# Kernel tuning notes

Measured on AMD Instinct MI355X. Metric: run time of the kernel, lower is better.

The kernel has to match this reference:

```python
import jax, jax.numpy as jnp
import numpy as np

N_NODES = 10000
N_EDGES = 320000
D_FEAT = 512
N_HIDDEN = 256
N_LATENT = 64


def setup_inputs() -> dict:
    key = jax.random.key(0)
    ks = jax.random.split(key, 7)
    x = jax.random.normal(ks[0], (N_NODES, D_FEAT), dtype=jnp.float32)
    edge_src = jax.random.randint(ks[1], (N_EDGES,), 0, N_NODES, dtype=jnp.int32)
    edge_dst = jax.random.randint(ks[2], (N_EDGES,), 0, N_NODES, dtype=jnp.int32)
    # positive weights, like D^{-1/2} A D^{-1/2} entries
    edge_weight = jax.random.uniform(ks[3], (N_EDGES,), dtype=jnp.float32)
    scale1 = 1.0 / np.sqrt(D_FEAT)
    scale2 = 1.0 / np.sqrt(N_HIDDEN)
    W1 = jax.random.normal(ks[4], (D_FEAT, N_HIDDEN), dtype=jnp.float32) * scale1
    W2_mu = jax.random.normal(ks[5], (N_HIDDEN, N_LATENT), dtype=jnp.float32) * scale2
    W2_sig = jax.random.normal(ks[6], (N_HIDDEN, N_LATENT), dtype=jnp.float32) * scale2
    return {"x": x, "edge_src": edge_src, "edge_dst": edge_dst,
            "edge_weight": edge_weight, "W1": W1, "W2_mu": W2_mu, "W2_sig": W2_sig}


def reference(x, edge_src, edge_dst, edge_weight, W1, W2_mu, W2_sig):
    N = x.shape[0]

    def spmm(feat):
        # sparse adj_norm @ feat via gather + weighted segment-sum
        msg = feat[edge_src] * edge_weight[:, None]           # [E, F]
        return jax.ops.segment_sum(msg, edge_dst, num_segments=N)  # [N, F]

    # GCN layer 1: relu(adj @ (x @ W1)); dropout is identity at inference
    h = jax.nn.relu(spmm(x @ W1))                              # [N, H]
    # GCN layer 2 (mu and log-sigma heads); encoder returns exp(log_sig)
    mu = spmm(h @ W2_mu)                                       # [N, L]
    sigma = jnp.exp(spmm(h @ W2_sig))                          # [N, L]
    # InnerProductDecoder: adj = z @ z.T (normalized z_ is computed but unused
    # in the original code, so it is faithfully omitted); z = mu embedding
    adj_rec = mu @ mu.T                                        # [N, N]
    return mu, sigma, adj_rec
```

## Files before the change

kernel.cpp:

```cpp
#include <hip/hip_runtime.h>
#include <hip/hip_bf16.h>
#include <math.h>
#include <float.h>

#define N_NODES 10000
#define N_EDGES 320000
#define D_FEAT  512
#define N_HID   256
#define N_LAT   64

typedef __bf16 bf16x2 __attribute__((ext_vector_type(2)));
typedef __bf16 bf16x4 __attribute__((ext_vector_type(4)));
typedef __bf16 bf16x8 __attribute__((ext_vector_type(8)));
typedef float  f32x2  __attribute__((ext_vector_type(2)));
typedef float  f32x4  __attribute__((ext_vector_type(4)));


__global__ __launch_bounds__(256) void k_hist8(const int* __restrict__ dst,
                                               int* __restrict__ deg8) {
    int i = blockIdx.x * 256 + threadIdx.x;
    int sh = blockIdx.x & 7;
    if (i < N_EDGES) atomicAdd(&deg8[sh * N_NODES + dst[i]], 1);
}

__global__ __launch_bounds__(1024) void k_scan8(const int* __restrict__ deg8,
                                                int* __restrict__ rowptr,
                                                int* __restrict__ woff8) {
    __shared__ int wsum[16];
    __shared__ int carry_s;
    int tid = threadIdx.x;
    if (tid == 0) carry_s = 0;
    __syncthreads();
    int lane = tid & 63, wv = tid >> 6;
    for (int base = 0; base < N_NODES; base += 1024) {
        int i = base + tid;
        int d8[8];
        int v = 0;
        #pragma unroll
        for (int s = 0; s < 8; s++) {
            d8[s] = (i < N_NODES) ? deg8[s * N_NODES + i] : 0;
            v += d8[s];
        }
        int x = v;
        #pragma unroll
        for (int off = 1; off < 64; off <<= 1) {
            int y = __shfl_up(x, off);
            if (lane >= off) x += y;
        }
        if (lane == 63) wsum[wv] = x;
        __syncthreads();
        int add = carry_s;
        for (int k = 0; k < wv; k++) add += wsum[k];
        int incl = x + add;
        int excl = incl - v;
        if (i < N_NODES) {
            rowptr[i] = excl;
            int run = excl;
            #pragma unroll
            for (int s = 0; s < 8; s++) { woff8[s * N_NODES + i] = run; run += d8[s]; }
        }
        __syncthreads();
        if (tid == 1023) carry_s = incl;
        __syncthreads();
    }
    if (tid == 0) rowptr[N_NODES] = carry_s;
}

__global__ __launch_bounds__(256) void k_scatter8(const int* __restrict__ src,
                                                  const int* __restrict__ dst,
                                                  const float* __restrict__ w,
                                                  int* __restrict__ woff8,
                                                  int* __restrict__ esrc,
                                                  float* __restrict__ ew) {
    int i = blockIdx.x * 256 + threadIdx.x;
    int sh = blockIdx.x & 7;
    if (i < N_EDGES) {
        int d = dst[i];
        int r = atomicAdd(&woff8[sh * N_NODES + d], 1);
        esrc[r] = src[i];
        ew[r] = w[i];
    }
}


__global__ __launch_bounds__(256) void k_split(const float* __restrict__ x,
                                               const float* __restrict__ W1,
                                               const float* __restrict__ W2mu,
                                               const float* __restrict__ W2sig,
                                               __bf16* __restrict__ xh,
                                               __bf16* __restrict__ xl,
                                               __bf16* __restrict__ w1h,
                                               __bf16* __restrict__ w1l,
                                               __bf16* __restrict__ w2h,
                                               __bf16* __restrict__ w2l) {
    if (blockIdx.x < 5000) {
        int i = blockIdx.x * 256 + threadIdx.x;
        float4 v = ((const float4*)x)[i];
        __bf16 h0 = (__bf16)v.x, h1 = (__bf16)v.y, h2 = (__bf16)v.z, h3 = (__bf16)v.w;
        bf16x4 hv = {h0, h1, h2, h3};
        bf16x4 lv = {(__bf16)(v.x - (float)h0), (__bf16)(v.y - (float)h1),
                     (__bf16)(v.z - (float)h2), (__bf16)(v.w - (float)h3)};
        ((bf16x4*)xh)[i] = hv;
        ((bf16x4*)xl)[i] = lv;
    } else {
        int i = (blockIdx.x - 5000) * 256 + threadIdx.x;
        if (i < 512 * 256) {
            int j = i >> 9, k = i & 511;
            float v = W1[k * N_HID + j];
            __bf16 hi = (__bf16)v;
            w1h[i] = hi;
            w1l[i] = (__bf16)(v - (float)hi);
        } else {
            int t = i - 512 * 256;
            int j = t >> 8, k = t & 255;
            float v = (j < 64) ? W2mu[k * N_LAT + j] : W2sig[k * N_LAT + (j - 64)];
            __bf16 hi = (__bf16)v;
            w2h[t] = hi;
            w2l[t] = (__bf16)(v - (float)hi);
        }
    }
}


__global__ __launch_bounds__(256) void k_gemm1m(const __bf16* __restrict__ xh,
                                                const __bf16* __restrict__ xl,
                                                const __bf16* __restrict__ w1h,
                                                const __bf16* __restrict__ w1l,
                                                float* __restrict__ xw1) {
    int tid = threadIdx.x;
    int l = tid & 63, w = tid >> 6;
    int wr = w >> 1, wc = w & 1;
    int i0 = blockIdx.y * 128 + wr * 64;
    int j0 = blockIdx.x * 64 + wc * 32;
    int lr = l & 15, lk = (l >> 4) * 8;

    f32x4 acc[4][2];
    #pragma unroll
    for (int a = 0; a < 4; a++)
        #pragma unroll
        for (int b = 0; b < 2; b++) acc[a][b] = (f32x4)(0.0f);

    #pragma unroll 4
    for (int ks = 0; ks < 16; ks++) {
        int k0 = ks * 32 + lk;
        bf16x8 ah[4], al[4], bh[2], bl[2];
        #pragma unroll
        for (int mi = 0; mi < 4; mi++) {
            int row = i0 + mi * 16 + lr;
            if (row > N_NODES - 1) row = N_NODES - 1;
            ah[mi] = *(const bf16x8*)(xh + row * D_FEAT + k0);
            al[mi] = *(const bf16x8*)(xl + row * D_FEAT + k0);
        }
        #pragma unroll
        for (int ni = 0; ni < 2; ni++) {
            int jr = j0 + ni * 16 + lr;
            bh[ni] = *(const bf16x8*)(w1h + jr * D_FEAT + k0);
            bl[ni] = *(const bf16x8*)(w1l + jr * D_FEAT + k0);
        }
        #pragma unroll
        for (int mi = 0; mi < 4; mi++)
            #pragma unroll
            for (int ni = 0; ni < 2; ni++) {
                acc[mi][ni] = __builtin_amdgcn_mfma_f32_16x16x32_bf16(ah[mi], bh[ni], acc[mi][ni], 0, 0, 0);
                acc[mi][ni] = __builtin_amdgcn_mfma_f32_16x16x32_bf16(ah[mi], bl[ni], acc[mi][ni], 0, 0, 0);
                acc[mi][ni] = __builtin_amdgcn_mfma_f32_16x16x32_bf16(al[mi], bh[ni], acc[mi][ni], 0, 0, 0);
            }
    }
    int c16 = l & 15, r4 = l >> 4;
    #pragma unroll
    for (int mi = 0; mi < 4; mi++)
        #pragma unroll
        for (int ni = 0; ni < 2; ni++)
            #pragma unroll
            for (int r = 0; r < 4; r++) {
                int row = i0 + mi * 16 + r4 * 4 + r;
                int col = j0 + ni * 16 + c16;
                if (row < N_NODES) xw1[row * N_HID + col] = acc[mi][ni][r];
            }
}


__global__ __launch_bounds__(256) void k_spmm1w(const int* __restrict__ rowptr,
                                                const int* __restrict__ esrc,
                                                const float* __restrict__ ew,
                                                const float* __restrict__ xw1,
                                                __bf16* __restrict__ hh,
                                                __bf16* __restrict__ hl) {
    int lane = threadIdx.x & 63, w = threadIdx.x >> 6;
    int n = blockIdx.x * 4 + w;
    int s = __builtin_amdgcn_readfirstlane(rowptr[n]);
    int e = __builtin_amdgcn_readfirstlane(rowptr[n + 1]);
    const float4* X = (const float4*)xw1;
    float4 acc = make_float4(0.f, 0.f, 0.f, 0.f);
    int i = s;
    for (; i + 3 < e; i += 4) {
        int s0 = esrc[i], s1 = esrc[i + 1], s2 = esrc[i + 2], s3 = esrc[i + 3];
        float w0 = ew[i], w1 = ew[i + 1], w2 = ew[i + 2], w3 = ew[i + 3];
        float4 v0 = X[s0 * 64 + lane];
        float4 v1 = X[s1 * 64 + lane];
        float4 v2 = X[s2 * 64 + lane];
        float4 v3 = X[s3 * 64 + lane];
        acc.x += w0 * v0.x + w1 * v1.x + w2 * v2.x + w3 * v3.x;
        acc.y += w0 * v0.y + w1 * v1.y + w2 * v2.y + w3 * v3.y;
        acc.z += w0 * v0.z + w1 * v1.z + w2 * v2.z + w3 * v3.z;
        acc.w += w0 * v0.w + w1 * v1.w + w2 * v2.w + w3 * v3.w;
    }
    for (; i < e; i++) {
        int sc = esrc[i]; float wv = ew[i];
        float4 v = X[sc * 64 + lane];
        acc.x += wv * v.x; acc.y += wv * v.y; acc.z += wv * v.z; acc.w += wv * v.w;
    }
    acc.x = fmaxf(acc.x, 0.f); acc.y = fmaxf(acc.y, 0.f);
    acc.z = fmaxf(acc.z, 0.f); acc.w = fmaxf(acc.w, 0.f);
    __bf16 h0 = (__bf16)acc.x, h1 = (__bf16)acc.y, h2 = (__bf16)acc.z, h3 = (__bf16)acc.w;
    bf16x4 hv = {h0, h1, h2, h3};
    bf16x4 lv = {(__bf16)(acc.x - (float)h0), (__bf16)(acc.y - (float)h1),
                 (__bf16)(acc.z - (float)h2), (__bf16)(acc.w - (float)h3)};
    ((bf16x4*)(hh + n * N_HID))[lane] = hv;
    ((bf16x4*)(hl + n * N_HID))[lane] = lv;
}


__global__ __launch_bounds__(256) void k_gemm2m(const __bf16* __restrict__ hh,
                                                const __bf16* __restrict__ hl,
                                                const __bf16* __restrict__ w2h,
                                                const __bf16* __restrict__ w2l,
                                                float* __restrict__ pre) {
    int tid = threadIdx.x;
    int l = tid & 63, w = tid >> 6;
    int wr = w >> 1, wc = w & 1;
    int i0 = blockIdx.y * 128 + wr * 64;
    int j0 = blockIdx.x * 64 + wc * 32;
    int lr = l & 15, lk = (l >> 4) * 8;

    f32x4 acc[4][2];
    #pragma unroll
    for (int a = 0; a < 4; a++)
        #pragma unroll
        for (int b = 0; b < 2; b++) acc[a][b] = (f32x4)(0.0f);

    #pragma unroll 4
    for (int ks = 0; ks < 8; ks++) {
        int k0 = ks * 32 + lk;
        bf16x8 ah[4], al[4], bh[2], bl[2];
        #pragma unroll
        for (int mi = 0; mi < 4; mi++) {
            int row = i0 + mi * 16 + lr;
            if (row > N_NODES - 1) row = N_NODES - 1;
            ah[mi] = *(const bf16x8*)(hh + row * N_HID + k0);
            al[mi] = *(const bf16x8*)(hl + row * N_HID + k0);
        }
        #pragma unroll
        for (int ni = 0; ni < 2; ni++) {
            int jr = j0 + ni * 16 + lr;
            bh[ni] = *(const bf16x8*)(w2h + jr * N_HID + k0);
            bl[ni] = *(const bf16x8*)(w2l + jr * N_HID + k0);
        }
        #pragma unroll
        for (int mi = 0; mi < 4; mi++)
            #pragma unroll
            for (int ni = 0; ni < 2; ni++) {
                acc[mi][ni] = __builtin_amdgcn_mfma_f32_16x16x32_bf16(ah[mi], bh[ni], acc[mi][ni], 0, 0, 0);
                acc[mi][ni] = __builtin_amdgcn_mfma_f32_16x16x32_bf16(ah[mi], bl[ni], acc[mi][ni], 0, 0, 0);
                acc[mi][ni] = __builtin_amdgcn_mfma_f32_16x16x32_bf16(al[mi], bh[ni], acc[mi][ni], 0, 0, 0);
            }
    }
    int c16 = l & 15, r4 = l >> 4;
    #pragma unroll
    for (int mi = 0; mi < 4; mi++)
        #pragma unroll
        for (int ni = 0; ni < 2; ni++)
            #pragma unroll
            for (int r = 0; r < 4; r++) {
                int row = i0 + mi * 16 + r4 * 4 + r;
                int col = j0 + ni * 16 + c16;
                if (row < N_NODES) pre[row * 128 + col] = acc[mi][ni][r];
            }
}


__global__ __launch_bounds__(256) void k_spmm2w(const int* __restrict__ rowptr,
                                                const int* __restrict__ esrc,
                                                const float* __restrict__ ew,
                                                const float* __restrict__ pre,
                                                float* __restrict__ out_mu,
                                                float* __restrict__ out_sig,
                                                __bf16* __restrict__ muh,
                                                __bf16* __restrict__ mul) {
    int lane = threadIdx.x & 63, w = threadIdx.x >> 6;
    int n = blockIdx.x * 4 + w;
    int s = __builtin_amdgcn_readfirstlane(rowptr[n]);
    int e = __builtin_amdgcn_readfirstlane(rowptr[n + 1]);
    const float2* P = (const float2*)pre;
    float2 acc = make_float2(0.f, 0.f);
    int i = s;
    for (; i + 3 < e; i += 4) {
        int s0 = esrc[i], s1 = esrc[i + 1], s2 = esrc[i + 2], s3 = esrc[i + 3];
        float w0 = ew[i], w1 = ew[i + 1], w2 = ew[i + 2], w3 = ew[i + 3];
        float2 v0 = P[s0 * 64 + lane];
        float2 v1 = P[s1 * 64 + lane];
        float2 v2 = P[s2 * 64 + lane];
        float2 v3 = P[s3 * 64 + lane];
        acc.x += w0 * v0.x + w1 * v1.x + w2 * v2.x + w3 * v3.x;
        acc.y += w0 * v0.y + w1 * v1.y + w2 * v2.y + w3 * v3.y;
    }
    for (; i < e; i++) {
        int sc = esrc[i]; float wv = ew[i];
        float2 v = P[sc * 64 + lane];
        acc.x += wv * v.x; acc.y += wv * v.y;
    }
    if (lane < 32) {
        f32x2 mv = {acc.x, acc.y};
        __builtin_nontemporal_store(mv, (f32x2*)(out_mu + n * 64) + lane);
        __bf16 h0 = (__bf16)acc.x, h1 = (__bf16)acc.y;
        bf16x2 hv = {h0, h1};
        bf16x2 lv = {(__bf16)(acc.x - (float)h0), (__bf16)(acc.y - (float)h1)};
        ((bf16x2*)(muh + n * 64))[lane] = hv;
        ((bf16x2*)(mul + n * 64))[lane] = lv;
    } else {
        f32x2 sg = {fminf(expf(acc.x), 3.0e38f), fminf(expf(acc.y), 3.0e38f)};
        __builtin_nontemporal_store(sg, (f32x2*)(out_sig + n * 64) + (lane - 32));
    }
}


#define ADJ_TS 68
#define ADJ_NB 6241
#define ADJ_Q  780
#define ADJ_R  1

__global__ __launch_bounds__(256) void k_adj(const __bf16* __restrict__ muh,
                                             const __bf16* __restrict__ mul,
                                             float* __restrict__ C) {
    __shared__ float Ts[4][32 * ADJ_TS];
    int g = blockIdx.x;
    int xcd = g & 7, idx = g >> 3;
    int wg = (xcd < ADJ_R ? xcd * (ADJ_Q + 1) : ADJ_R * (ADJ_Q + 1) + (xcd - ADJ_R) * ADJ_Q) + idx;
    int ti = wg / 79, tj = wg % 79;

    int tid = threadIdx.x;
    int l = tid & 63, w = tid >> 6;
    int wr = w >> 1, wc = w & 1;
    int i0 = ti * 128 + wr * 64;
    int j0 = tj * 128 + wc * 64;
    int lr = l & 15;
    int lk = (l >> 4) * 8;

    f32x4 acc[4][4];
    #pragma unroll
    for (int a = 0; a < 4; a++)
        #pragma unroll
        for (int b = 0; b < 4; b++) acc[a][b] = (f32x4)(0.0f);

    #pragma unroll
    for (int ks = 0; ks < 2; ks++) {
        int k0 = ks * 32 + lk;
        bf16x8 ah[4], al[4], bh[4], bl[4];
        #pragma unroll
        for (int mi = 0; mi < 4; mi++) {
            int row = i0 + mi * 16 + lr;
            if (row > N_NODES - 1) row = N_NODES - 1;
            ah[mi] = *(const bf16x8*)(muh + row * 64 + k0);
            al[mi] = *(const bf16x8*)(mul + row * 64 + k0);
        }
        #pragma unroll
        for (int ni = 0; ni < 4; ni++) {
            int row = j0 + ni * 16 + lr;
            if (row > N_NODES - 1) row = N_NODES - 1;
            bh[ni] = *(const bf16x8*)(muh + row * 64 + k0);
            bl[ni] = *(const bf16x8*)(mul + row * 64 + k0);
        }
        #pragma unroll
        for (int mi = 0; mi < 4; mi++)
            #pragma unroll
            for (int ni = 0; ni < 4; ni++) {
                acc[mi][ni] = __builtin_amdgcn_mfma_f32_16x16x32_bf16(ah[mi], bh[ni], acc[mi][ni], 0, 0, 0);
                acc[mi][ni] = __builtin_amdgcn_mfma_f32_16x16x32_bf16(ah[mi], bl[ni], acc[mi][ni], 0, 0, 0);
                acc[mi][ni] = __builtin_amdgcn_mfma_f32_16x16x32_bf16(al[mi], bh[ni], acc[mi][ni], 0, 0, 0);
            }
    }

    float* T = Ts[w];
    int c16 = l & 15, r4 = l >> 4;
    #pragma unroll
    for (int half = 0; half < 2; half++) {
        __syncthreads();
        #pragma unroll
        for (int m2 = 0; m2 < 2; m2++) {
            int mi = half * 2 + m2;
            #pragma unroll
            for (int ni = 0; ni < 4; ni++)
                #pragma unroll
                for (int r = 0; r < 4; r++)
                    T[(m2 * 16 + r4 * 4 + r) * ADJ_TS + ni * 16 + c16] = acc[mi][ni][r];
        }
        __syncthreads();
        #pragma unroll
        for (int q = 0; q < 8; q++) {
            int rr = q * 4 + r4;
            int row = i0 + half * 32 + rr;
            int col = j0 + c16 * 4;
            if (row < N_NODES && col < N_NODES) {
                f32x4 val = *(const f32x4*)&T[rr * ADJ_TS + c16 * 4];
                __builtin_nontemporal_store(val, (f32x4*)&C[(size_t)row * N_NODES + col]);
            }
        }
    }
}


extern "C" void kernel_launch(void* const* d_in, const int* in_sizes, int n_in,
                              void* d_out, int out_size, void* d_ws, size_t ws_size,
                              hipStream_t stream) {
    const float* x       = (const float*)d_in[0];
    const int*   esrc_in = (const int*)d_in[1];
    const int*   edst_in = (const int*)d_in[2];
    const float* ew_in   = (const float*)d_in[3];
    const float* W1      = (const float*)d_in[4];
    const float* W2mu    = (const float*)d_in[5];
    const float* W2sig   = (const float*)d_in[6];

    char* ws = (char*)d_ws;
    __bf16* xh   = (__bf16*)(ws + 0);
    __bf16* xl   = (__bf16*)(ws + 10240000);
    float*  xw1  = (float*) (ws + 20480000);
    __bf16* hh   = (__bf16*)(ws + 0);
    __bf16* hl   = (__bf16*)(ws + 5120000);
    float*  pre  = (float*) (ws + 10240000);
    __bf16* muh  = (__bf16*)(ws + 20480000);
    __bf16* mul  = (__bf16*)(ws + 21760000);
    int*    esrc = (int*)   (ws + 30720000);
    float*  ew   = (float*) (ws + 32000000);
    __bf16* w1h  = (__bf16*)(ws + 33280000);
    __bf16* w1l  = (__bf16*)(ws + 33542144);
    __bf16* w2h  = (__bf16*)(ws + 33804288);
    __bf16* w2l  = (__bf16*)(ws + 33869824);
    int*  rowptr = (int*)   (ws + 33935360);
    int*    deg8 = (int*)   (ws + 33975376);
    int*   woff8 = (int*)   (ws + 34295376);

    float* out_mu  = (float*)d_out;
    float* out_sig = out_mu + 640000;
    float* out_adj = out_sig + 640000;

    hipMemsetAsync(deg8, 0, 8 * N_NODES * sizeof(int), stream);
    k_hist8   <<<(N_EDGES + 255) / 256, 256, 0, stream>>>(edst_in, deg8);
    k_scan8   <<<1, 1024, 0, stream>>>(deg8, rowptr, woff8);
    k_scatter8<<<(N_EDGES + 255) / 256, 256, 0, stream>>>(esrc_in, edst_in, ew_in,
                                                          woff8, esrc, ew);
    k_split   <<<5640, 256, 0, stream>>>(x, W1, W2mu, W2sig, xh, xl, w1h, w1l, w2h, w2l);
    {
        dim3 g(4, (N_NODES + 127) / 128);
        k_gemm1m<<<g, 256, 0, stream>>>(xh, xl, w1h, w1l, xw1);
    }
    k_spmm1w  <<<N_NODES / 4, 256, 0, stream>>>(rowptr, esrc, ew, xw1, hh, hl);
    {
        dim3 g(2, (N_NODES + 127) / 128);
        k_gemm2m<<<g, 256, 0, stream>>>(hh, hl, w2h, w2l, pre);
    }
    k_spmm2w  <<<N_NODES / 4, 256, 0, stream>>>(rowptr, esrc, ew, pre,
                                                out_mu, out_sig, muh, mul);
    k_adj     <<<ADJ_NB, 256, 0, stream>>>(muh, mul, out_adj);
}
```

Before: 635.1 us.

## Merge independent kernels, unroll spmm1 gather, shrink gemm2 tiles, drop nontemporal stores

```diff
diff --git a/kernel.cpp b/kernel.cpp
--- a/kernel.cpp
+++ b/kernel.cpp
@@ -16,12 +16,54 @@
 typedef float  f32x4  __attribute__((ext_vector_type(4)));
 
 
-__global__ __launch_bounds__(256) void k_hist8(const int* __restrict__ dst,
-                                               int* __restrict__ deg8) {
-    int i = blockIdx.x * 256 + threadIdx.x;
-    int sh = blockIdx.x & 7;
-    if (i < N_EDGES) atomicAdd(&deg8[sh * N_NODES + dst[i]], 1);
-}
+__global__ __launch_bounds__(256) void k_hist_split(const int* __restrict__ dst,
+                                                    int* __restrict__ deg8,
+                                                    const float* __restrict__ x,
+                                                    const float* __restrict__ W1,
+                                                    const float* __restrict__ W2mu,
+                                                    const float* __restrict__ W2sig,
+                                                    __bf16* __restrict__ xh,
+                                                    __bf16* __restrict__ xl,
+                                                    __bf16* __restrict__ w1h,
+                                                    __bf16* __restrict__ w1l,
+                                                    __bf16* __restrict__ w2h,
+                                                    __bf16* __restrict__ w2l) {
+    int b = blockIdx.x;
+    if (b < 1250) {
+        int i = b * 256 + threadIdx.x;
+        int sh = b & 7;
+        if (i < N_EDGES) atomicAdd(&deg8[sh * N_NODES + dst[i]], 1);
+        return;
+    }
+    int bb = b - 1250;
+    if (bb < 5000) {
+        int i = bb * 256 + threadIdx.x;
+        float4 v = ((const float4*)x)[i];
+        __bf16 h0 = (__bf16)v.x, h1 = (__bf16)v.y, h2 = (__bf16)v.z, h3 = (__bf16)v.w;
+        bf16x4 hv = {h0, h1, h2, h3};
+        bf16x4 lv = {(__bf16)(v.x - (float)h0), (__bf16)(v.y - (float)h1),
+                     (__bf16)(v.z - (float)h2), (__bf16)(v.w - (float)h3)};
+        ((bf16x4*)xh)[i] = hv;
+        ((bf16x4*)xl)[i] = lv;
+    } else {
+        int i = (bb - 5000) * 256 + threadIdx.x;
+        if (i < 512 * 256) {
+            int j = i >> 9, k = i & 511;
+            float v = W1[k * N_HID + j];
+            __bf16 hi = (__bf16)v;
+            w1h[i] = hi;
+            w1l[i] = (__bf16)(v - (float)hi);
+        } else {
+            int t = i - 512 * 256;
+            int j = t >> 8, k = t & 255;
+            float v = (j < 64) ? W2mu[k * N_LAT + j] : W2sig[k * N_LAT + (j - 64)];
+            __bf16 hi = (__bf16)v;
+            w2h[t] = hi;
+            w2l[t] = (__bf16)(v - (float)hi);
+        }
+    }
+}
+
 
 __global__ __launch_bounds__(1024) void k_scan8(const int* __restrict__ deg8,
                                                 int* __restrict__ rowptr,
@@ -66,79 +108,44 @@
     if (tid == 0) rowptr[N_NODES] = carry_s;
 }
 
-__global__ __launch_bounds__(256) void k_scatter8(const int* __restrict__ src,
-                                                  const int* __restrict__ dst,
-                                                  const float* __restrict__ w,
-                                                  int* __restrict__ woff8,
-                                                  int* __restrict__ esrc,
-                                                  float* __restrict__ ew) {
-    int i = blockIdx.x * 256 + threadIdx.x;
-    int sh = blockIdx.x & 7;
-    if (i < N_EDGES) {
-        int d = dst[i];
-        int r = atomicAdd(&woff8[sh * N_NODES + d], 1);
-        esrc[r] = src[i];
-        ew[r] = w[i];
-    }
-}
-
-
-__global__ __launch_bounds__(256) void k_split(const float* __restrict__ x,
-                                               const float* __restrict__ W1,
-                                               const float* __restrict__ W2mu,
-                                               const float* __restrict__ W2sig,
-                                               __bf16* __restrict__ xh,
-                                               __bf16* __restrict__ xl,
-                                               __bf16* __restrict__ w1h,
-                                               __bf16* __restrict__ w1l,
-                                               __bf16* __restrict__ w2h,
-                                               __bf16* __restrict__ w2l) {
-    if (blockIdx.x < 5000) {
-        int i = blockIdx.x * 256 + threadIdx.x;
-        float4 v = ((const float4*)x)[i];
-        __bf16 h0 = (__bf16)v.x, h1 = (__bf16)v.y, h2 = (__bf16)v.z, h3 = (__bf16)v.w;
-        bf16x4 hv = {h0, h1, h2, h3};
-        bf16x4 lv = {(__bf16)(v.x - (float)h0), (__bf16)(v.y - (float)h1),
-                     (__bf16)(v.z - (float)h2), (__bf16)(v.w - (float)h3)};
-        ((bf16x4*)xh)[i] = hv;
-        ((bf16x4*)xl)[i] = lv;
-    } else {
-        int i = (blockIdx.x - 5000) * 256 + threadIdx.x;
-        if (i < 512 * 256) {
-            int j = i >> 9, k = i & 511;
-            float v = W1[k * N_HID + j];
-            __bf16 hi = (__bf16)v;
-            w1h[i] = hi;
-            w1l[i] = (__bf16)(v - (float)hi);
-        } else {
-            int t = i - 512 * 256;
-            int j = t >> 8, k = t & 255;
-            float v = (j < 64) ? W2mu[k * N_LAT + j] : W2sig[k * N_LAT + (j - 64)];
-            __bf16 hi = (__bf16)v;
-            w2h[t] = hi;
-            w2l[t] = (__bf16)(v - (float)hi);
-        }
-    }
-}
-
-
-__global__ __launch_bounds__(256) void k_gemm1m(const __bf16* __restrict__ xh,
-                                                const __bf16* __restrict__ xl,
-                                                const __bf16* __restrict__ w1h,
-                                                const __bf16* __restrict__ w1l,
-                                                float* __restrict__ xw1) {
+
+__global__ __launch_bounds__(256) void k_scat_gemm1(const int* __restrict__ src,
+                                                    const int* __restrict__ dst,
+                                                    const float* __restrict__ wgt,
+                                                    int* __restrict__ woff8,
+                                                    int* __restrict__ esrc,
+                                                    float* __restrict__ ew,
+                                                    const __bf16* __restrict__ xh,
+                                                    const __bf16* __restrict__ xl,
+                                                    const __bf16* __restrict__ w1h,
+                                                    const __bf16* __restrict__ w1l,
+                                                    float* __restrict__ xw1) {
+    int b = blockIdx.x;
+    if (b < 1250) {
+        int i = b * 256 + threadIdx.x;
+        int sh = b & 7;
+        if (i < N_EDGES) {
+            int d = dst[i];
+            int r = atomicAdd(&woff8[sh * N_NODES + d], 1);
+            esrc[r] = src[i];
+            ew[r] = wgt[i];
+        }
+        return;
+    }
+    int g = b - 1250;
+    int bx = g & 3, by = g >> 2;
     int tid = threadIdx.x;
     int l = tid & 63, w = tid >> 6;
     int wr = w >> 1, wc = w & 1;
-    int i0 = blockIdx.y * 128 + wr * 64;
-    int j0 = blockIdx.x * 64 + wc * 32;
+    int i0 = by * 128 + wr * 64;
+    int j0 = bx * 64 + wc * 32;
     int lr = l & 15, lk = (l >> 4) * 8;
 
     f32x4 acc[4][2];
     #pragma unroll
     for (int a = 0; a < 4; a++)
         #pragma unroll
-        for (int b = 0; b < 2; b++) acc[a][b] = (f32x4)(0.0f);
+        for (int c = 0; c < 2; c++) acc[a][c] = (f32x4)(0.0f);
 
     #pragma unroll 4
     for (int ks = 0; ks < 16; ks++) {
@@ -193,6 +200,20 @@
     const float4* X = (const float4*)xw1;
     float4 acc = make_float4(0.f, 0.f, 0.f, 0.f);
     int i = s;
+    for (; i + 7 < e; i += 8) {
+        int   ix[8];
+        float wv[8];
+        #pragma unroll
+        for (int u = 0; u < 8; u++) { ix[u] = esrc[i + u]; wv[u] = ew[i + u]; }
+        float4 v[8];
+        #pragma unroll
+        for (int u = 0; u < 8; u++) v[u] = X[ix[u] * 64 + lane];
+        #pragma unroll
+        for (int u = 0; u < 8; u++) {
+            acc.x += wv[u] * v[u].x; acc.y += wv[u] * v[u].y;
+            acc.z += wv[u] * v[u].z; acc.w += wv[u] * v[u].w;
+        }
+    }
     for (; i + 3 < e; i += 4) {
         int s0 = esrc[i], s1 = esrc[i + 1], s2 = esrc[i + 2], s3 = esrc[i + 3];
         float w0 = ew[i], w1 = ew[i + 1], w2 = ew[i + 2], w3 = ew[i + 3];
@@ -229,22 +250,22 @@
     int tid = threadIdx.x;
     int l = tid & 63, w = tid >> 6;
     int wr = w >> 1, wc = w & 1;
-    int i0 = blockIdx.y * 128 + wr * 64;
+    int i0 = blockIdx.y * 64 + wr * 32;
     int j0 = blockIdx.x * 64 + wc * 32;
     int lr = l & 15, lk = (l >> 4) * 8;
 
-    f32x4 acc[4][2];
-    #pragma unroll
-    for (int a = 0; a < 4; a++)
-        #pragma unroll
-        for (int b = 0; b < 2; b++) acc[a][b] = (f32x4)(0.0f);
+    f32x4 acc[2][2];
+    #pragma unroll
+    for (int a = 0; a < 2; a++)
+        #pragma unroll
+        for (int c = 0; c < 2; c++) acc[a][c] = (f32x4)(0.0f);
 
     #pragma unroll 4
     for (int ks = 0; ks < 8; ks++) {
         int k0 = ks * 32 + lk;
-        bf16x8 ah[4], al[4], bh[2], bl[2];
-        #pragma unroll
-        for (int mi = 0; mi < 4; mi++) {
+        bf16x8 ah[2], al[2], bh[2], bl[2];
+        #pragma unroll
+        for (int mi = 0; mi < 2; mi++) {
             int row = i0 + mi * 16 + lr;
             if (row > N_NODES - 1) row = N_NODES - 1;
             ah[mi] = *(const bf16x8*)(hh + row * N_HID + k0);
@@ -257,7 +278,7 @@
             bl[ni] = *(const bf16x8*)(w2l + jr * N_HID + k0);
         }
         #pragma unroll
-        for (int mi = 0; mi < 4; mi++)
+        for (int mi = 0; mi < 2; mi++)
             #pragma unroll
             for (int ni = 0; ni < 2; ni++) {
                 acc[mi][ni] = __builtin_amdgcn_mfma_f32_16x16x32_bf16(ah[mi], bh[ni], acc[mi][ni], 0, 0, 0);
@@ -267,7 +288,7 @@
     }
     int c16 = l & 15, r4 = l >> 4;
     #pragma unroll
-    for (int mi = 0; mi < 4; mi++)
+    for (int mi = 0; mi < 2; mi++)
         #pragma unroll
         for (int ni = 0; ni < 2; ni++)
             #pragma unroll
@@ -310,16 +331,16 @@
         acc.x += wv * v.x; acc.y += wv * v.y;
     }
     if (lane < 32) {
-        f32x2 mv = {acc.x, acc.y};
-        __builtin_nontemporal_store(mv, (f32x2*)(out_mu + n * 64) + lane);
+        ((float2*)(out_mu + n * 64))[lane] = acc;
         __bf16 h0 = (__bf16)acc.x, h1 = (__bf16)acc.y;
         bf16x2 hv = {h0, h1};
         bf16x2 lv = {(__bf16)(acc.x - (float)h0), (__bf16)(acc.y - (float)h1)};
         ((bf16x2*)(muh + n * 64))[lane] = hv;
         ((bf16x2*)(mul + n * 64))[lane] = lv;
     } else {
-        f32x2 sg = {fminf(expf(acc.x), 3.0e38f), fminf(expf(acc.y), 3.0e38f)};
-        __builtin_nontemporal_store(sg, (f32x2*)(out_sig + n * 64) + (lane - 32));
+        float2 sg = make_float2(fminf(expf(acc.x), 3.0e38f),
+                                fminf(expf(acc.y), 3.0e38f));
+        ((float2*)(out_sig + n * 64))[lane - 32] = sg;
     }
 }
 
@@ -350,7 +371,7 @@
     #pragma unroll
     for (int a = 0; a < 4; a++)
         #pragma unroll
-        for (int b = 0; b < 4; b++) acc[a][b] = (f32x4)(0.0f);
+        for (int c = 0; c < 4; c++) acc[a][c] = (f32x4)(0.0f);
 
     #pragma unroll
     for (int ks = 0; ks < 2; ks++) {
@@ -400,10 +421,9 @@
             int rr = q * 4 + r4;
             int row = i0 + half * 32 + rr;
             int col = j0 + c16 * 4;
-            if (row < N_NODES && col < N_NODES) {
-                f32x4 val = *(const f32x4*)&T[rr * ADJ_TS + c16 * 4];
-                __builtin_nontemporal_store(val, (f32x4*)&C[(size_t)row * N_NODES + col]);
-            }
+            if (row < N_NODES && col < N_NODES)
+                *(float4*)&C[(size_t)row * N_NODES + col] =
+                    *(const float4*)&T[rr * ADJ_TS + c16 * 4];
         }
     }
 }
@@ -444,21 +464,17 @@
     float* out_adj = out_sig + 640000;
 
     hipMemsetAsync(deg8, 0, 8 * N_NODES * sizeof(int), stream);
-    k_hist8   <<<(N_EDGES + 255) / 256, 256, 0, stream>>>(edst_in, deg8);
-    k_scan8   <<<1, 1024, 0, stream>>>(deg8, rowptr, woff8);
-    k_scatter8<<<(N_EDGES + 255) / 256, 256, 0, stream>>>(esrc_in, edst_in, ew_in,
-                                                          woff8, esrc, ew);
-    k_split   <<<5640, 256, 0, stream>>>(x, W1, W2mu, W2sig, xh, xl, w1h, w1l, w2h, w2l);
+    k_hist_split <<<1250 + 5640, 256, 0, stream>>>(edst_in, deg8, x, W1, W2mu, W2sig,
+                                                   xh, xl, w1h, w1l, w2h, w2l);
+    k_scan8      <<<1, 1024, 0, stream>>>(deg8, rowptr, woff8);
+    k_scat_gemm1 <<<1250 + 316, 256, 0, stream>>>(esrc_in, edst_in, ew_in, woff8,
+                                                  esrc, ew, xh, xl, w1h, w1l, xw1);
+    k_spmm1w     <<<N_NODES / 4, 256, 0, stream>>>(rowptr, esrc, ew, xw1, hh, hl);
     {
-        dim3 g(4, (N_NODES + 127) / 128);
-        k_gemm1m<<<g, 256, 0, stream>>>(xh, xl, w1h, w1l, xw1);
-    }
-    k_spmm1w  <<<N_NODES / 4, 256, 0, stream>>>(rowptr, esrc, ew, xw1, hh, hl);
-    {
-        dim3 g(2, (N_NODES + 127) / 128);
-        k_gemm2m<<<g, 256, 0, stream>>>(hh, hl, w2h, w2l, pre);
-    }
-    k_spmm2w  <<<N_NODES / 4, 256, 0, stream>>>(rowptr, esrc, ew, pre,
-                                                out_mu, out_sig, muh, mul);
-    k_adj     <<<ADJ_NB, 256, 0, stream>>>(muh, mul, out_adj);
-}
+        dim3 g(2, 157);
+        k_gemm2m <<<g, 256, 0, stream>>>(hh, hl, w2h, w2l, pre);
+    }
+    k_spmm2w     <<<N_NODES / 4, 256, 0, stream>>>(rowptr, esrc, ew, pre,
+                                                   out_mu, out_sig, muh, mul);
+    k_adj        <<<ADJ_NB, 256, 0, stream>>>(muh, mul, out_adj);
+}
```

Result: slower. 656.0 us (+3.3%).
